# Performance work log

Measured on AMD Instinct MI355X. Metric: run time of the kernel, lower is better.

Reference implementation:

```python
import jax, jax.numpy as jnp
import numpy as np

B, T, D_MODEL = 2, 2048, 2048
N_HEADS, N_KV = 16, 8
HEAD_DIM = D_MODEL // N_HEADS  # 128
EPS = 1e-6


def rmsnorm(x, g):
    # qwen-compatible: compute in fp32, scale by learned weight
    xf = x.astype(jnp.float32)
    var = jnp.mean(xf * xf, axis=-1, keepdims=True)
    return (xf * jax.lax.rsqrt(var + EPS) * g).astype(x.dtype)


def apply_rope(x, cos, sin):
    # x: [b, h, t, d]; cos/sin: [t, d]
    d = x.shape[-1]
    x1, x2 = x[..., : d // 2], x[..., d // 2 :]
    rotated = jnp.concatenate([-x2, x1], axis=-1)
    return x * cos[None, None, :, :] + rotated * sin[None, None, :, :]


def setup_inputs() -> dict:
    key = jax.random.key(0)
    ks = jax.random.split(key, 8)
    x = jax.random.normal(ks[0], (B, T, D_MODEL), dtype=jnp.float32)
    # causal mask: True = masked out
    mask = jnp.triu(jnp.ones((T, T), dtype=bool), k=1)
    # rope tables
    inv_freq = 1.0 / (1e6 ** (np.arange(0, HEAD_DIM, 2, dtype=np.float32) / HEAD_DIM))
    angles = np.arange(T, dtype=np.float32)[:, None] * inv_freq[None, :]  # [T, d/2]
    angles = np.concatenate([angles, angles], axis=1)  # [T, d]
    cos = jnp.asarray(np.cos(angles), dtype=jnp.float32)
    sin = jnp.asarray(np.sin(angles), dtype=jnp.float32)
    s = 0.02
    Wq = jax.random.normal(ks[1], (D_MODEL, D_MODEL), dtype=jnp.float32) * s
    Wk = jax.random.normal(ks[2], (N_KV * HEAD_DIM, D_MODEL), dtype=jnp.float32) * s
    Wv = jax.random.normal(ks[3], (N_KV * HEAD_DIM, D_MODEL), dtype=jnp.float32) * s
    Wo = jax.random.normal(ks[4], (D_MODEL, D_MODEL), dtype=jnp.float32) * s
    bo = jnp.zeros((D_MODEL,), dtype=jnp.float32)
    gq = jnp.ones((HEAD_DIM,), dtype=jnp.float32)
    gk = jnp.ones((HEAD_DIM,), dtype=jnp.float32)
    return {"x": x, "mask": mask, "cos": cos, "sin": sin, "Wq": Wq, "Wk": Wk,
            "Wv": Wv, "Wo": Wo, "bo": bo, "gq": gq, "gk": gk}


def reference(x, mask, cos, sin, Wq, Wk, Wv, Wo, bo, gq, gk):
    b, t, _ = x.shape
    # projections
    q = (x @ Wq.T).reshape(b, t, N_HEADS, HEAD_DIM)
    q = rmsnorm(q, gq).transpose(0, 2, 1, 3)          # [b, H, t, d]
    q = apply_rope(q, cos[:t], sin[:t])
    k = (x @ Wk.T).reshape(b, t, N_KV, HEAD_DIM)
    k = rmsnorm(k, gk).transpose(0, 2, 1, 3)          # [b, G, t, d]
    k = apply_rope(k, cos[:t], sin[:t])
    v = (x @ Wv.T).reshape(b, t, N_KV, HEAD_DIM).transpose(0, 2, 1, 3)
    # GQA broadcast of KV heads
    rep = N_HEADS // N_KV
    k = jnp.repeat(k, rep, axis=1)                    # [b, H, t, d]
    v = jnp.repeat(v, rep, axis=1)
    scores = jnp.einsum("bhqd,bhkd->bhqk", q, k)
    scores = jnp.where(mask[:t, :t][None, None], -jnp.inf, scores)
    attn = jax.nn.softmax(scores / jnp.sqrt(jnp.float32(HEAD_DIM)), axis=-1)
    out = jnp.einsum("bhqk,bhkd->bqhd", attn, v).reshape(b, t, N_HEADS * HEAD_DIM)
    return out @ Wo.T + bo
```

## Files before the change

kernel.cpp:

```cpp
#include <hip/hip_runtime.h>
#include <stdint.h>

#define B_ 2
#define T_ 2048
#define DM 2048
#define NH 16
#define NKV 8
#define HD 128
#define NQKV 4096
#define SC2_ 0.12753102765f

typedef float fx4 __attribute__((ext_vector_type(4)));
typedef __bf16 bfx8 __attribute__((ext_vector_type(8)));
typedef unsigned short u16;
typedef unsigned int u32;

typedef __attribute__((address_space(1))) const void gas_t;
typedef __attribute__((address_space(3))) void las_t;

__device__ __forceinline__ u16 f2bf(float f) {
  u32 u = __float_as_uint(f);
  u = (u + 0x7fffu + ((u >> 16) & 1u)) >> 16;
  return (u16)u;
}

__device__ __forceinline__ void stage16(const void* g, void* l) {
  __builtin_amdgcn_global_load_lds((gas_t*)(uintptr_t)g, (las_t*)(uintptr_t)l,
                                   16, 0, 0);
}

__global__ void k_cvt(const float* __restrict__ in, u16* __restrict__ out, int n) {
  int i = (blockIdx.x * blockDim.x + threadIdx.x) * 4;
  if (i + 3 < n) {
    float4 v = *(const float4*)(in + i);
    u32 w0 = (u32)f2bf(v.x) | ((u32)f2bf(v.y) << 16);
    u32 w1 = (u32)f2bf(v.z) | ((u32)f2bf(v.w) << 16);
    *(uint2*)(out + i) = make_uint2(w0, w1);
  }
}

__global__ __launch_bounds__(512, 2) void k_gemm256(const u16* __restrict__ A,
                                                    const u16* __restrict__ Bm,
                                                    u16* __restrict__ C,
                                                    int M, int N, int K) {
  __shared__ __align__(16) u16 As[2][2][256 * 32];
  __shared__ __align__(16) u16 Bs[2][2][256 * 32];
  const int nbn = N >> 8;
  const int bm = blockIdx.x / nbn, bn = blockIdx.x % nbn;
  const int tid = threadIdx.x;
  const int w = tid >> 6, lane = tid & 63;
  const int wm = w >> 2, wn = w & 3;
  const int lr = lane & 15, lg = lane >> 4;
  const int cw = (lg ^ ((lr >> 1) & 3)) * 8;
  const u16* Ab = A + (size_t)bm * 256 * K;
  const u16* Bb = Bm + (size_t)bn * 256 * K;
  const int NT = K >> 6;

  auto stage = [&](const u16* gb, u16* region, int tile, int kh) {
#pragma unroll
    for (int i = 0; i < 2; i++) {
      int q = tid + i * 512;
      int row = q >> 2, ch = q & 3;
      int sc = ch ^ ((row >> 1) & 3);
      stage16(gb + (size_t)row * K + tile * 64 + kh * 32 + sc * 8, region + q * 8);
    }
  };

  fx4 acc[8][4];
  const fx4 zero4 = {0.f, 0.f, 0.f, 0.f};
#pragma unroll
  for (int m = 0; m < 8; m++)
#pragma unroll
    for (int n = 0; n < 4; n++) acc[m][n] = zero4;

  stage(Ab, &As[0][0][0], 0, 0);
  stage(Bb, &Bs[0][0][0], 0, 0);
  stage(Ab, &As[0][1][0], 0, 1);
  stage(Bb, &Bs[0][1][0], 0, 1);
  stage(Ab, &As[1][0][0], 1, 0);
  stage(Bb, &Bs[1][0][0], 1, 0);
  asm volatile("s_waitcnt vmcnt(4)" ::: "memory");
  __builtin_amdgcn_s_barrier();

  const int arow = (wm * 128 + lr) * 32;
  const int brow = (wn * 64 + lr) * 32;
  bfx8 af[4], bf[4];

#pragma unroll 1
  for (int t = 0; t < NT; t++) {
    const u16* A0 = &As[t & 1][0][0];
    const u16* A1 = &As[t & 1][1][0];
    const u16* B0 = &Bs[t & 1][0][0];
    const u16* B1 = &Bs[t & 1][1][0];
    const int p1 = (t + 1) & 1, p2 = t & 1;

#pragma unroll
    for (int mi = 0; mi < 4; mi++) af[mi] = *(const bfx8*)(A0 + arow + mi * 512 + cw);
#pragma unroll
    for (int n = 0; n < 4; n++) bf[n] = *(const bfx8*)(B0 + brow + n * 512 + cw);
    if (t + 1 < NT) stage(Ab, &As[p1][1][0], t + 1, 1);
    __builtin_amdgcn_s_barrier();
    asm volatile("s_waitcnt lgkmcnt(0)" ::: "memory");
    __builtin_amdgcn_sched_barrier(0);
    __builtin_amdgcn_s_setprio(1);
#pragma unroll
    for (int mi = 0; mi < 4; mi++)
#pragma unroll
      for (int n = 0; n < 4; n++)
        acc[mi][n] = __builtin_amdgcn_mfma_f32_16x16x32_bf16(af[mi], bf[n], acc[mi][n], 0, 0, 0);
    __builtin_amdgcn_s_setprio(0);
    __builtin_amdgcn_s_barrier();

#pragma unroll
    for (int mi = 0; mi < 4; mi++)
      af[mi] = *(const bfx8*)(A0 + arow + 2048 + mi * 512 + cw);
    if (t + 1 < NT) stage(Bb, &Bs[p1][1][0], t + 1, 1);
    __builtin_amdgcn_s_barrier();
    asm volatile("s_waitcnt lgkmcnt(0)" ::: "memory");
    __builtin_amdgcn_sched_barrier(0);
    __builtin_amdgcn_s_setprio(1);
#pragma unroll
    for (int mi = 0; mi < 4; mi++)
#pragma unroll
      for (int n = 0; n < 4; n++)
        acc[4 + mi][n] = __builtin_amdgcn_mfma_f32_16x16x32_bf16(af[mi], bf[n], acc[4 + mi][n], 0, 0, 0);
    __builtin_amdgcn_s_setprio(0);
    __builtin_amdgcn_s_barrier();

#pragma unroll
    for (int mi = 0; mi < 4; mi++) af[mi] = *(const bfx8*)(A1 + arow + mi * 512 + cw);
#pragma unroll
    for (int n = 0; n < 4; n++) bf[n] = *(const bfx8*)(B1 + brow + n * 512 + cw);
    if (t + 2 < NT) stage(Ab, &As[p2][0][0], t + 2, 0);
    __builtin_amdgcn_s_barrier();
    asm volatile("s_waitcnt lgkmcnt(0)" ::: "memory");
    __builtin_amdgcn_sched_barrier(0);
    __builtin_amdgcn_s_setprio(1);
#pragma unroll
    for (int mi = 0; mi < 4; mi++)
#pragma unroll
      for (int n = 0; n < 4; n++)
        acc[mi][n] = __builtin_amdgcn_mfma_f32_16x16x32_bf16(af[mi], bf[n], acc[mi][n], 0, 0, 0);
    __builtin_amdgcn_s_setprio(0);
    __builtin_amdgcn_s_barrier();

#pragma unroll
    for (int mi = 0; mi < 4; mi++)
      af[mi] = *(const bfx8*)(A1 + arow + 2048 + mi * 512 + cw);
    if (t + 2 < NT) stage(Bb, &Bs[p2][0][0], t + 2, 0);
    __builtin_amdgcn_s_barrier();
    asm volatile("s_waitcnt lgkmcnt(0)" ::: "memory");
    __builtin_amdgcn_sched_barrier(0);
    __builtin_amdgcn_s_setprio(1);
#pragma unroll
    for (int mi = 0; mi < 4; mi++)
#pragma unroll
      for (int n = 0; n < 4; n++)
        acc[4 + mi][n] = __builtin_amdgcn_mfma_f32_16x16x32_bf16(af[mi], bf[n], acc[4 + mi][n], 0, 0, 0);
    __builtin_amdgcn_s_setprio(0);
    asm volatile("s_waitcnt vmcnt(4)" ::: "memory");
    __builtin_amdgcn_s_barrier();
  }

  const int r0 = bm * 256 + wm * 128, c0 = bn * 256 + wn * 64;
#pragma unroll
  for (int m = 0; m < 8; m++) {
#pragma unroll
    for (int n = 0; n < 4; n++) {
      int c = c0 + n * 16 + lr;
#pragma unroll
      for (int i = 0; i < 4; i++)
        C[(size_t)(r0 + m * 16 + lg * 4 + i) * N + c] = f2bf(acc[m][n][i]);
    }
  }
}

template <bool OUT_F32>
__global__ __launch_bounds__(256, 2) void k_gemm(const u16* __restrict__ A,
                                                 const u16* __restrict__ Bm,
                                                 void* __restrict__ Cv,
                                                 const float* __restrict__ bias,
                                                 int M, int N, int K) {
  __shared__ __align__(16) u16 As[128 * 32];
  __shared__ __align__(16) u16 Bs[128 * 32];
  const int nbn = N >> 7;
  const int bm = blockIdx.x / nbn, bn = blockIdx.x % nbn;
  const int tid = threadIdx.x;
  const int w = tid >> 6, lane = tid & 63;
  const int wr = w >> 1, wc = w & 1;
  const int lr = lane & 15, lg = lane >> 4;
  const u16* Ab = A + (size_t)bm * 128 * K;
  const u16* Bb = Bm + (size_t)bn * 128 * K;
  const int srow = lane >> 2, skc = (lane & 3) * 8;

  fx4 zero4 = {0.f, 0.f, 0.f, 0.f};
  fx4 acc[4][4];
#pragma unroll
  for (int m = 0; m < 4; m++)
#pragma unroll
    for (int n = 0; n < 4; n++) acc[m][n] = zero4;

  for (int k0 = 0; k0 < K; k0 += 32) {
#pragma unroll
    for (int t = 0; t < 2; t++) {
      int s = w + t * 4;
      stage16(Ab + (size_t)(s * 16 + srow) * K + k0 + skc, As + s * 512 + lane * 8);
      stage16(Bb + (size_t)(s * 16 + srow) * K + k0 + skc, Bs + s * 512 + lane * 8);
    }
    __syncthreads();
    bfx8 af[4], bfr[4];
#pragma unroll
    for (int m = 0; m < 4; m++)
      af[m] = *(const bfx8*)(As + (wr * 64 + m * 16 + lr) * 32 + lg * 8);
#pragma unroll
    for (int n = 0; n < 4; n++)
      bfr[n] = *(const bfx8*)(Bs + (wc * 64 + n * 16 + lr) * 32 + lg * 8);
#pragma unroll
    for (int m = 0; m < 4; m++)
#pragma unroll
      for (int n = 0; n < 4; n++)
        acc[m][n] = __builtin_amdgcn_mfma_f32_16x16x32_bf16(af[m], bfr[n], acc[m][n], 0, 0, 0);
    __syncthreads();
  }

  const int r0 = bm * 128 + wr * 64, c0 = bn * 128 + wc * 64;
#pragma unroll
  for (int m = 0; m < 4; m++) {
#pragma unroll
    for (int n = 0; n < 4; n++) {
      int c = c0 + n * 16 + lr;
#pragma unroll
      for (int i = 0; i < 4; i++) {
        int r = r0 + m * 16 + lg * 4 + i;
        if (OUT_F32) {
          ((float*)Cv)[(size_t)r * N + c] = acc[m][n][i] + bias[c];
        } else {
          ((u16*)Cv)[(size_t)r * N + c] = f2bf(acc[m][n][i]);
        }
      }
    }
  }
}

__global__ __launch_bounds__(256) void k_qkpost(const u16* __restrict__ qkv,
                                                const float* __restrict__ cosp,
                                                const float* __restrict__ sinp,
                                                const float* __restrict__ gq,
                                                const float* __restrict__ gk,
                                                u16* __restrict__ Qo,
                                                u16* __restrict__ Ko) {
  int bi = blockIdx.x;
  int hh = bi % 24;
  int t64 = (bi / 24) % 32;
  int b = bi / 768;
  int tid = threadIdx.x;
  int j = tid >> 2, p = tid & 3;
  int t = t64 * 64 + j;
  bool isq = hh < 16;
  int colbase = isq ? hh * 128 : 2048 + (hh - 16) * 128;
  const u16* src = qkv + ((size_t)(b * T_ + t)) * NQKV + colbase + p * 32;

  float xv[32];
#pragma unroll
  for (int c = 0; c < 4; c++) {
    uint4 raw = *(const uint4*)(src + c * 8);
    u32 wd[4] = {raw.x, raw.y, raw.z, raw.w};
#pragma unroll
    for (int q2 = 0; q2 < 4; q2++) {
      xv[c * 8 + q2 * 2 + 0] = __uint_as_float(wd[q2] << 16);
      xv[c * 8 + q2 * 2 + 1] = __uint_as_float(wd[q2] & 0xffff0000u);
    }
  }
  float ss = 0.f;
#pragma unroll
  for (int i = 0; i < 32; i++) ss += xv[i] * xv[i];
  ss += __shfl_xor(ss, 1);
  ss += __shfl_xor(ss, 2);
  float rinv = rsqrtf(ss * (1.0f / 128.0f) + 1e-6f);
  const float* g = isq ? gq : gk;
  const float* cr = cosp + (size_t)t * 128 + p * 32;
  const float* sr = sinp + (size_t)t * 128 + p * 32;

  float ov[32];
#pragma unroll
  for (int i = 0; i < 32; i++) {
    float y = xv[i] * rinv * g[p * 32 + i];
    float oth = __shfl_xor(y, 2);
    float rot = (p < 2) ? -oth : oth;
    ov[i] = y * cr[i] + rot * sr[i];
  }

  uint4 pk[4];
#pragma unroll
  for (int c = 0; c < 4; c++) {
    u32 wd[4];
#pragma unroll
    for (int q2 = 0; q2 < 4; q2++)
      wd[q2] = (u32)f2bf(ov[c * 8 + q2 * 2]) | ((u32)f2bf(ov[c * 8 + q2 * 2 + 1]) << 16);
    pk[c] = make_uint4(wd[0], wd[1], wd[2], wd[3]);
  }

  if (isq) {
    u16* dst = Qo + (((size_t)(b * NH + hh)) * T_ + t) * HD + p * 32;
#pragma unroll
    for (int c = 0; c < 4; c++) *(uint4*)(dst + c * 8) = pk[c];
  } else {
    int hk = hh - 16;
    u16* dstrow = Ko + (((size_t)(b * NKV + hk)) * T_ + t) * HD;
#pragma unroll
    for (int c = 0; c < 4; c++) {
      int C = p * 4 + c;
      int Cs = C ^ (t & 7);
      *(uint4*)(dstrow + Cs * 8) = pk[c];
    }
  }
}

__global__ __launch_bounds__(256) void k_vtr(const u16* __restrict__ qkv,
                                             u16* __restrict__ vt) {
  __shared__ __align__(16) u16 sm[128 * 64];
  int bi = blockIdx.x;
  int hv = bi & 7;
  int t64 = (bi >> 3) & 31;
  int b = bi >> 8;
  int tid = threadIdx.x;
#pragma unroll
  for (int it = 0; it < 4; it++) {
    int idx = tid + it * 256;
    int tok = idx >> 4, c = idx & 15;
    uint4 raw = *(const uint4*)(qkv + ((size_t)(b * T_ + t64 * 64 + tok)) * NQKV +
                                3072 + hv * 128 + c * 8);
    u32 wd[4] = {raw.x, raw.y, raw.z, raw.w};
#pragma unroll
    for (int q2 = 0; q2 < 4; q2++) {
      sm[(c * 8 + q2 * 2 + 0) * 64 + tok] = (u16)(wd[q2] & 0xffffu);
      sm[(c * 8 + q2 * 2 + 1) * 64 + tok] = (u16)(wd[q2] >> 16);
    }
  }
  __syncthreads();
  int d = tid >> 1, half = tid & 1;
  size_t rowb = (((size_t)(b * NKV + hv)) * HD + d) * T_ + t64 * 64;
#pragma unroll
  for (int c = 0; c < 4; c++) {
    int cg = half * 4 + c;
    int cs = cg ^ (d & 7);
    u32 wd[4];
#pragma unroll
    for (int q2 = 0; q2 < 4; q2++) {
      u32 lo = sm[d * 64 + half * 32 + c * 8 + 2 * q2];
      u32 hi = sm[d * 64 + half * 32 + c * 8 + 2 * q2 + 1];
      wd[q2] = lo | (hi << 16);
    }
    *(uint4*)(vt + rowb + cs * 8) = make_uint4(wd[0], wd[1], wd[2], wd[3]);
  }
}

__global__ __launch_bounds__(512, 4) void k_attn(const u16* __restrict__ Qg,
                                                 const u16* __restrict__ Kg,
                                                 const u16* __restrict__ Vg,
                                                 u16* __restrict__ Og) {
  __shared__ __align__(16) u16 Ks[2][64 * 128];
  __shared__ __align__(16) u16 Vs[2][128 * 64];
  __shared__ __align__(16) u16 Ps[8][16 * 64];
  const int bi = blockIdx.x;
  const int zr = bi & 15, h = (bi >> 4) & 15, b = bi >> 8;
  const int z = b ? (15 - zr) : zr;
  const int hkv = h >> 1;
  const int tid = threadIdx.x, w = tid >> 6, lane = tid & 63;
  const int lr = lane & 15, lg = lane >> 4;
  const int zt = (w < 4) ? z : (31 - z);
  const int qr0 = zt * 64 + (w & 3) * 16;
  const int nch = 32 - z;
  const int myl = zt + 1;

  const u16* kb = Kg + ((size_t)(b * NKV + hkv)) * T_ * HD;
  const u16* vb = Vg + ((size_t)(b * NKV + hkv)) * HD * T_;
  u16* pw = &Ps[w][0];
  const fx4 zero4 = {0.f, 0.f, 0.f, 0.f};

  auto stageKV = [&](int buf, int kv0) {
    u16* Kd = &Ks[buf][0];
    u16* Vd = &Vs[buf][0];
#pragma unroll
    for (int it = 0; it < 2; it++) {
      int r = it * 32 + (tid >> 4);
      stage16(kb + (size_t)(kv0 + r) * HD + (tid & 15) * 8, Kd + it * 4096 + tid * 8);
      int d = it * 64 + (tid >> 3);
      stage16(vb + (size_t)d * T_ + kv0 + (tid & 7) * 8, Vd + it * 4096 + tid * 8);
    }
  };

  const u16* qbase = Qg + (((size_t)(b * NH + h)) * T_ + qr0 + lr) * HD;
  bfx8 qf[4];
#pragma unroll
  for (int kk = 0; kk < 4; kk++) qf[kk] = *(const bfx8*)(qbase + kk * 32 + lg * 8);

  fx4 o[8];
#pragma unroll
  for (int nf = 0; nf < 8; nf++) o[nf] = zero4;
  float l_i[4] = {0.f, 0.f, 0.f, 0.f};

  stageKV(0, 0);
  asm volatile("s_waitcnt vmcnt(0)" ::: "memory");
  __builtin_amdgcn_s_barrier();
  int cur = 0;

#pragma unroll 1
  for (int ch = 0; ch < nch; ch++) {
    if (ch + 1 < nch) {
      stageKV(cur ^ 1, (ch + 1) * 64);
      asm volatile("s_waitcnt vmcnt(4)" ::: "memory");
    } else {
      asm volatile("s_waitcnt vmcnt(0)" ::: "memory");
    }
    __builtin_amdgcn_s_barrier();

    if (ch < myl) {
      const u16* Kd = &Ks[cur][0];
      const u16* Vd = &Vs[cur][0];
      const int kv0 = ch * 64;
      const bool diag = (ch == zt);

      fx4 sa[4];
#pragma unroll
      for (int n = 0; n < 4; n++) sa[n] = zero4;
      __builtin_amdgcn_s_setprio(1);
#pragma unroll
      for (int n = 0; n < 4; n++) {
        const int kvl = n * 16 + lr;
        const u16* krow = Kd + kvl * 128;
#pragma unroll
        for (int kk = 0; kk < 4; kk++) {
          int cs = (kk * 4 + lg) ^ (kvl & 7);
          bfx8 kf = *(const bfx8*)(krow + cs * 8);
          sa[n] = __builtin_amdgcn_mfma_f32_16x16x32_bf16(qf[kk], kf, sa[n], 0, 0, 0);
        }
      }
      __builtin_amdgcn_s_setprio(0);

#pragma unroll
      for (int i = 0; i < 4; i++) {
        const int q = 4 * lg + i;
        const int r = qr0 + q;
        u16* prow = pw + q * 64;
#pragma unroll
        for (int n = 0; n < 4; n++) {
          float p = exp2f(sa[n][i] * SC2_);
          if (diag) p = ((kv0 + n * 16 + lr) > r) ? 0.f : p;
          l_i[i] += p;
          int chn = ((n * 2 + (lr >> 3)) ^ (q & 7));
          prow[chn * 8 + (lr & 7)] = f2bf(p);
        }
      }
      asm volatile("s_waitcnt lgkmcnt(0)" ::: "memory");

      bfx8 pa[2];
#pragma unroll
      for (int ks = 0; ks < 2; ks++) {
        int cp = (4 * ks + lg) ^ (lr & 7);
        pa[ks] = *(const bfx8*)(pw + lr * 64 + cp * 8);
      }
      __builtin_amdgcn_s_setprio(1);
#pragma unroll
      for (int nf = 0; nf < 8; nf++) {
        int d = nf * 16 + lr;
        const u16* vrow = Vd + d * 64;
#pragma unroll
        for (int ks = 0; ks < 2; ks++) {
          int cv = (4 * ks + lg) ^ (d & 7);
          bfx8 vf = *(const bfx8*)(vrow + cv * 8);
          o[nf] = __builtin_amdgcn_mfma_f32_16x16x32_bf16(pa[ks], vf, o[nf], 0, 0, 0);
        }
      }
      __builtin_amdgcn_s_setprio(0);
    }
    __builtin_amdgcn_s_barrier();
    cur ^= 1;
  }

  float inv[4];
#pragma unroll
  for (int i = 0; i < 4; i++) {
    float l = l_i[i];
    l += __shfl_xor(l, 1);
    l += __shfl_xor(l, 2);
    l += __shfl_xor(l, 4);
    l += __shfl_xor(l, 8);
    inv[i] = 1.0f / l;
  }
  u16* ob = Og + ((size_t)(b * T_ + qr0)) * DM + h * HD;
#pragma unroll
  for (int nf = 0; nf < 8; nf++)
#pragma unroll
    for (int i = 0; i < 4; i++)
      ob[(size_t)(4 * lg + i) * DM + nf * 16 + lr] = f2bf(o[nf][i] * inv[i]);
}

extern "C" void kernel_launch(void* const* d_in, const int* in_sizes, int n_in,
                              void* d_out, int out_size, void* d_ws, size_t ws_size,
                              hipStream_t stream) {
  const float* x = (const float*)d_in[0];
  const float* cosp = (const float*)d_in[2];
  const float* sinp = (const float*)d_in[3];
  const float* Wq = (const float*)d_in[4];
  const float* Wk = (const float*)d_in[5];
  const float* Wv = (const float*)d_in[6];
  const float* Wo = (const float*)d_in[7];
  const float* bo = (const float*)d_in[8];
  const float* gq = (const float*)d_in[9];
  const float* gk = (const float*)d_in[10];

  char* ws = (char*)d_ws;
  u16* xbf  = (u16*)(ws + 0);
  u16* wqkv = (u16*)(ws + 16777216);
  u16* wo   = (u16*)(ws + 33554432);
  u16* qkv  = (u16*)(ws + 41943040);
  u16* qb   = (u16*)(ws + 75497472);
  u16* kb   = (u16*)(ws + 92274688);
  u16* vt   = (u16*)(ws + 100663296);
  u16* ab   = (u16*)(ws + 109051904);
  float* out = (float*)d_out;

  k_cvt<<<8192, 256, 0, stream>>>(x, xbf, 8388608);
  k_cvt<<<4096, 256, 0, stream>>>(Wq, wqkv, 4194304);
  k_cvt<<<2048, 256, 0, stream>>>(Wk, wqkv + 4194304, 2097152);
  k_cvt<<<2048, 256, 0, stream>>>(Wv, wqkv + 6291456, 2097152);
  k_cvt<<<4096, 256, 0, stream>>>(Wo, wo, 4194304);

  k_gemm256<<<256, 512, 0, stream>>>(xbf, wqkv, qkv, 4096, 4096, 2048);
  k_qkpost<<<1536, 256, 0, stream>>>(qkv, cosp, sinp, gq, gk, qb, kb);
  k_vtr<<<512, 256, 0, stream>>>(qkv, vt);
  k_attn<<<512, 512, 0, stream>>>(qb, kb, vt, ab);
  k_gemm<true><<<512, 256, 0, stream>>>(ab, wo, out, bo, 4096, 2048, 2048);
}
```

Before: 248.8 us.

## Rewrite attention with 32x32 MFMA and register-resident P via permlane swap

The attention kernel moves from 16x16x32 to 32x32x16 bf16 MFMA tiles, with each wave owning 32 query rows, and the block shrinks from 512 to 256 threads. The computed S^T layout lets P be packed to bf16 and rearranged with v_permlane32_swap so it feeds the PV MFMA straight from registers, which removes the per-wave LDS round trip for P. Query-tile selection is also reshuffled across waves. The aim is less LDS traffic and fewer MFMA instructions, at the cost of more registers per wave and fewer waves per block sharing the same KV staging.

```diff
diff --git a/kernel.cpp b/kernel.cpp
--- a/kernel.cpp
+++ b/kernel.cpp
@@ -11,7 +11,9 @@
 #define SC2_ 0.12753102765f
 
 typedef float fx4 __attribute__((ext_vector_type(4)));
+typedef float fx16 __attribute__((ext_vector_type(16)));
 typedef __bf16 bfx8 __attribute__((ext_vector_type(8)));
+typedef unsigned int ux4 __attribute__((ext_vector_type(4)));
 typedef unsigned short u16;
 typedef unsigned int u32;
 
@@ -22,6 +24,9 @@
   u32 u = __float_as_uint(f);
   u = (u + 0x7fffu + ((u >> 16) & 1u)) >> 16;
   return (u16)u;
+}
+__device__ __forceinline__ u32 pk2bf(float lo, float hi) {
+  return (u32)f2bf(lo) | ((u32)f2bf(hi) << 16);
 }
 
 __device__ __forceinline__ void stage16(const void* g, void* l) {
@@ -355,50 +360,52 @@
   }
 }
 
-__global__ __launch_bounds__(512, 4) void k_attn(const u16* __restrict__ Qg,
+__global__ __launch_bounds__(256, 2) void k_attn(const u16* __restrict__ Qg,
                                                  const u16* __restrict__ Kg,
                                                  const u16* __restrict__ Vg,
                                                  u16* __restrict__ Og) {
   __shared__ __align__(16) u16 Ks[2][64 * 128];
   __shared__ __align__(16) u16 Vs[2][128 * 64];
-  __shared__ __align__(16) u16 Ps[8][16 * 64];
   const int bi = blockIdx.x;
   const int zr = bi & 15, h = (bi >> 4) & 15, b = bi >> 8;
   const int z = b ? (15 - zr) : zr;
   const int hkv = h >> 1;
   const int tid = threadIdx.x, w = tid >> 6, lane = tid & 63;
-  const int lr = lane & 15, lg = lane >> 4;
-  const int zt = (w < 4) ? z : (31 - z);
-  const int qr0 = zt * 64 + (w & 3) * 16;
+  const int q31 = lane & 31, H8 = lane >> 5;
+  const int sel = ((w >> 1) ^ bi) & 1;
+  const int zt = sel ? (31 - z) : z;
+  const int qr0 = zt * 64 + (w & 1) * 32;
+  const int qg = qr0 + q31;
   const int nch = 32 - z;
   const int myl = zt + 1;
 
   const u16* kb = Kg + ((size_t)(b * NKV + hkv)) * T_ * HD;
   const u16* vb = Vg + ((size_t)(b * NKV + hkv)) * HD * T_;
-  u16* pw = &Ps[w][0];
-  const fx4 zero4 = {0.f, 0.f, 0.f, 0.f};
+
+  const u16* qrow = Qg + (((size_t)(b * NH + h)) * T_ + qg) * HD;
+  bfx8 qf[8];
+#pragma unroll
+  for (int step = 0; step < 8; step++)
+    qf[step] = *(const bfx8*)(qrow + step * 16 + H8 * 8);
+
+  fx16 o[4];
+  const fx16 zero16 = {0.f, 0.f, 0.f, 0.f, 0.f, 0.f, 0.f, 0.f,
+                       0.f, 0.f, 0.f, 0.f, 0.f, 0.f, 0.f, 0.f};
+#pragma unroll
+  for (int db = 0; db < 4; db++) o[db] = zero16;
+  float l_i = 0.f;
 
   auto stageKV = [&](int buf, int kv0) {
     u16* Kd = &Ks[buf][0];
     u16* Vd = &Vs[buf][0];
 #pragma unroll
-    for (int it = 0; it < 2; it++) {
-      int r = it * 32 + (tid >> 4);
-      stage16(kb + (size_t)(kv0 + r) * HD + (tid & 15) * 8, Kd + it * 4096 + tid * 8);
-      int d = it * 64 + (tid >> 3);
-      stage16(vb + (size_t)d * T_ + kv0 + (tid & 7) * 8, Vd + it * 4096 + tid * 8);
+    for (int it = 0; it < 4; it++) {
+      int r = it * 16 + (tid >> 4);
+      stage16(kb + (size_t)(kv0 + r) * HD + (tid & 15) * 8, Kd + it * 2048 + tid * 8);
+      int d = it * 32 + (tid >> 3);
+      stage16(vb + (size_t)d * T_ + kv0 + (tid & 7) * 8, Vd + it * 2048 + tid * 8);
     }
   };
-
-  const u16* qbase = Qg + (((size_t)(b * NH + h)) * T_ + qr0 + lr) * HD;
-  bfx8 qf[4];
-#pragma unroll
-  for (int kk = 0; kk < 4; kk++) qf[kk] = *(const bfx8*)(qbase + kk * 32 + lg * 8);
-
-  fx4 o[8];
-#pragma unroll
-  for (int nf = 0; nf < 8; nf++) o[nf] = zero4;
-  float l_i[4] = {0.f, 0.f, 0.f, 0.f};
 
   stageKV(0, 0);
   asm volatile("s_waitcnt vmcnt(0)" ::: "memory");
@@ -409,7 +416,7 @@
   for (int ch = 0; ch < nch; ch++) {
     if (ch + 1 < nch) {
       stageKV(cur ^ 1, (ch + 1) * 64);
-      asm volatile("s_waitcnt vmcnt(4)" ::: "memory");
+      asm volatile("s_waitcnt vmcnt(8)" ::: "memory");
     } else {
       asm volatile("s_waitcnt vmcnt(0)" ::: "memory");
     }
@@ -421,79 +428,73 @@
       const int kv0 = ch * 64;
       const bool diag = (ch == zt);
 
-      fx4 sa[4];
-#pragma unroll
-      for (int n = 0; n < 4; n++) sa[n] = zero4;
-      __builtin_amdgcn_s_setprio(1);
-#pragma unroll
-      for (int n = 0; n < 4; n++) {
-        const int kvl = n * 16 + lr;
-        const u16* krow = Kd + kvl * 128;
-#pragma unroll
-        for (int kk = 0; kk < 4; kk++) {
-          int cs = (kk * 4 + lg) ^ (kvl & 7);
-          bfx8 kf = *(const bfx8*)(krow + cs * 8);
-          sa[n] = __builtin_amdgcn_mfma_f32_16x16x32_bf16(qf[kk], kf, sa[n], 0, 0, 0);
+#pragma unroll
+      for (int kvb = 0; kvb < 2; kvb++) {
+        const int krow = kvb * 32 + q31;
+        const u16* kr = Kd + krow * 128;
+        fx16 st = zero16;
+        __builtin_amdgcn_s_setprio(1);
+#pragma unroll
+        for (int step = 0; step < 8; step++) {
+          int cs = ((step << 1) | H8) ^ (krow & 7);
+          bfx8 kf = *(const bfx8*)(kr + cs * 8);
+          st = __builtin_amdgcn_mfma_f32_32x32x16_bf16(kf, qf[step], st, 0, 0, 0);
+        }
+        __builtin_amdgcn_s_setprio(0);
+
+        float pv[16];
+#pragma unroll
+        for (int r = 0; r < 16; r++) {
+          float p = exp2f(st[r] * SC2_);
+          if (diag) {
+            int kvg = kv0 + kvb * 32 + (r & 3) + 8 * (r >> 2) + 4 * H8;
+            p = (kvg > qg) ? 0.f : p;
+          }
+          l_i += p;
+          pv[r] = p;
+        }
+
+#pragma unroll
+        for (int half = 0; half < 2; half++) {
+          const int rb = half * 8;
+          u32 A0 = pk2bf(pv[rb + 0], pv[rb + 1]);
+          u32 A1 = pk2bf(pv[rb + 2], pv[rb + 3]);
+          u32 B0 = pk2bf(pv[rb + 4], pv[rb + 5]);
+          u32 B1 = pk2bf(pv[rb + 6], pv[rb + 7]);
+          asm volatile("v_permlane32_swap_b32 %0, %1" : "+v"(A0), "+v"(B0));
+          asm volatile("v_permlane32_swap_b32 %0, %1" : "+v"(A1), "+v"(B1));
+          union { ux4 u; bfx8 b; } pa;
+          pa.u = (ux4){A0, A1, B0, B1};
+          const int ks = kvb * 2 + half;
+          __builtin_amdgcn_s_setprio(1);
+#pragma unroll
+          for (int db = 0; db < 4; db++) {
+            int vrow = db * 32 + q31;
+            int cv = ((ks << 1) | H8) ^ (vrow & 7);
+            bfx8 vf = *(const bfx8*)(Vd + vrow * 64 + cv * 8);
+            o[db] = __builtin_amdgcn_mfma_f32_32x32x16_bf16(vf, pa.b, o[db], 0, 0, 0);
+          }
+          __builtin_amdgcn_s_setprio(0);
         }
       }
-      __builtin_amdgcn_s_setprio(0);
-
-#pragma unroll
-      for (int i = 0; i < 4; i++) {
-        const int q = 4 * lg + i;
-        const int r = qr0 + q;
-        u16* prow = pw + q * 64;
-#pragma unroll
-        for (int n = 0; n < 4; n++) {
-          float p = exp2f(sa[n][i] * SC2_);
-          if (diag) p = ((kv0 + n * 16 + lr) > r) ? 0.f : p;
-          l_i[i] += p;
-          int chn = ((n * 2 + (lr >> 3)) ^ (q & 7));
-          prow[chn * 8 + (lr & 7)] = f2bf(p);
-        }
-      }
-      asm volatile("s_waitcnt lgkmcnt(0)" ::: "memory");
-
-      bfx8 pa[2];
-#pragma unroll
-      for (int ks = 0; ks < 2; ks++) {
-        int cp = (4 * ks + lg) ^ (lr & 7);
-        pa[ks] = *(const bfx8*)(pw + lr * 64 + cp * 8);
-      }
-      __builtin_amdgcn_s_setprio(1);
-#pragma unroll
-      for (int nf = 0; nf < 8; nf++) {
-        int d = nf * 16 + lr;
-        const u16* vrow = Vd + d * 64;
-#pragma unroll
-        for (int ks = 0; ks < 2; ks++) {
-          int cv = (4 * ks + lg) ^ (d & 7);
-          bfx8 vf = *(const bfx8*)(vrow + cv * 8);
-          o[nf] = __builtin_amdgcn_mfma_f32_16x16x32_bf16(pa[ks], vf, o[nf], 0, 0, 0);
-        }
-      }
-      __builtin_amdgcn_s_setprio(0);
     }
     __builtin_amdgcn_s_barrier();
     cur ^= 1;
   }
 
-  float inv[4];
-#pragma unroll
-  for (int i = 0; i < 4; i++) {
-    float l = l_i[i];
-    l += __shfl_xor(l, 1);
-    l += __shfl_xor(l, 2);
-    l += __shfl_xor(l, 4);
-    l += __shfl_xor(l, 8);
-    inv[i] = 1.0f / l;
-  }
-  u16* ob = Og + ((size_t)(b * T_ + qr0)) * DM + h * HD;
-#pragma unroll
-  for (int nf = 0; nf < 8; nf++)
-#pragma unroll
-    for (int i = 0; i < 4; i++)
-      ob[(size_t)(4 * lg + i) * DM + nf * 16 + lr] = f2bf(o[nf][i] * inv[i]);
+  float lt = l_i + __shfl_xor(l_i, 32);
+  float inv = 1.0f / lt;
+  u16* ob = Og + ((size_t)(b * T_ + qg)) * DM + h * HD;
+#pragma unroll
+  for (int db = 0; db < 4; db++) {
+#pragma unroll
+    for (int g = 0; g < 4; g++) {
+      int d0 = db * 32 + 8 * g + 4 * H8;
+      u32 w0 = pk2bf(o[db][4 * g + 0] * inv, o[db][4 * g + 1] * inv);
+      u32 w1 = pk2bf(o[db][4 * g + 2] * inv, o[db][4 * g + 3] * inv);
+      *(uint2*)(ob + d0) = make_uint2(w0, w1);
+    }
+  }
 }
 
 extern "C" void kernel_launch(void* const* d_in, const int* in_sizes, int n_in,
@@ -530,6 +531,6 @@
   k_gemm256<<<256, 512, 0, stream>>>(xbf, wqkv, qkv, 4096, 4096, 2048);
   k_qkpost<<<1536, 256, 0, stream>>>(qkv, cosp, sinp, gq, gk, qb, kb);
   k_vtr<<<512, 256, 0, stream>>>(qkv, vt);
-  k_attn<<<512, 512, 0, stream>>>(qb, kb, vt, ab);
+  k_attn<<<512, 256, 0, stream>>>(qb, kb, vt, ab);
   k_gemm<true><<<512, 256, 0, stream>>>(ab, wo, out, bo, 4096, 2048, 2048);
 }
```

Result: slower. 267.2 us (+7.4%).

## Pipeline output projection GEMM with double-buffered swizzled LDS and async prefetch

Applied to the files above, without the earlier changes.

Replaces the simple synchronous output-projection GEMM with a version modelled on the 256-tile QKV GEMM. It uses double-buffered LDS tiles with K split in halves, an XOR-swizzled LDS layout, and staged global prefetch interleaved with the MFMA phases. This is meant to overlap the global loads with compute and to cut bank conflicts and barrier stalls. It also adds a full vmcnt(0) drain on the last iterations of both GEMMs so no loads are left outstanding at the tail. The cost is a larger LDS footprint of 64KB per block, which may limit occupancy at two blocks per CU.

```diff
diff --git a/kernel.cpp b/kernel.cpp
--- a/kernel.cpp
+++ b/kernel.cpp
@@ -158,7 +158,11 @@
       for (int n = 0; n < 4; n++)
         acc[4 + mi][n] = __builtin_amdgcn_mfma_f32_16x16x32_bf16(af[mi], bf[n], acc[4 + mi][n], 0, 0, 0);
     __builtin_amdgcn_s_setprio(0);
-    asm volatile("s_waitcnt vmcnt(4)" ::: "memory");
+    if (t + 2 < NT) {
+      asm volatile("s_waitcnt vmcnt(4)" ::: "memory");
+    } else {
+      asm volatile("s_waitcnt vmcnt(0)" ::: "memory");
+    }
     __builtin_amdgcn_s_barrier();
   }
 
@@ -175,69 +179,143 @@
   }
 }
 
-template <bool OUT_F32>
-__global__ __launch_bounds__(256, 2) void k_gemm(const u16* __restrict__ A,
-                                                 const u16* __restrict__ Bm,
-                                                 void* __restrict__ Cv,
-                                                 const float* __restrict__ bias,
-                                                 int M, int N, int K) {
-  __shared__ __align__(16) u16 As[128 * 32];
-  __shared__ __align__(16) u16 Bs[128 * 32];
+__global__ __launch_bounds__(256, 2) void k_gemmo(const u16* __restrict__ A,
+                                                  const u16* __restrict__ Bm,
+                                                  float* __restrict__ C,
+                                                  const float* __restrict__ bias,
+                                                  int M, int N, int K) {
+  __shared__ __align__(16) u16 As[2][2][128 * 32];
+  __shared__ __align__(16) u16 Bs[2][2][128 * 32];
   const int nbn = N >> 7;
   const int bm = blockIdx.x / nbn, bn = blockIdx.x % nbn;
   const int tid = threadIdx.x;
   const int w = tid >> 6, lane = tid & 63;
-  const int wr = w >> 1, wc = w & 1;
+  const int wm = w >> 1, wn = w & 1;
   const int lr = lane & 15, lg = lane >> 4;
+  const int cw = (lg ^ ((lr >> 1) & 3)) * 8;
   const u16* Ab = A + (size_t)bm * 128 * K;
   const u16* Bb = Bm + (size_t)bn * 128 * K;
-  const int srow = lane >> 2, skc = (lane & 3) * 8;
-
-  fx4 zero4 = {0.f, 0.f, 0.f, 0.f};
+  const int NT = K >> 6;
+
+  auto stage = [&](const u16* gb, u16* region, int tile, int kh) {
+#pragma unroll
+    for (int i = 0; i < 2; i++) {
+      int q = tid + i * 256;
+      int row = q >> 2, ch = q & 3;
+      int sc = ch ^ ((row >> 1) & 3);
+      stage16(gb + (size_t)row * K + tile * 64 + kh * 32 + sc * 8, region + q * 8);
+    }
+  };
+
   fx4 acc[4][4];
+  const fx4 zero4 = {0.f, 0.f, 0.f, 0.f};
 #pragma unroll
   for (int m = 0; m < 4; m++)
 #pragma unroll
     for (int n = 0; n < 4; n++) acc[m][n] = zero4;
 
-  for (int k0 = 0; k0 < K; k0 += 32) {
-#pragma unroll
-    for (int t = 0; t < 2; t++) {
-      int s = w + t * 4;
-      stage16(Ab + (size_t)(s * 16 + srow) * K + k0 + skc, As + s * 512 + lane * 8);
-      stage16(Bb + (size_t)(s * 16 + srow) * K + k0 + skc, Bs + s * 512 + lane * 8);
-    }
-    __syncthreads();
-    bfx8 af[4], bfr[4];
-#pragma unroll
-    for (int m = 0; m < 4; m++)
-      af[m] = *(const bfx8*)(As + (wr * 64 + m * 16 + lr) * 32 + lg * 8);
-#pragma unroll
-    for (int n = 0; n < 4; n++)
-      bfr[n] = *(const bfx8*)(Bs + (wc * 64 + n * 16 + lr) * 32 + lg * 8);
-#pragma unroll
-    for (int m = 0; m < 4; m++)
-#pragma unroll
-      for (int n = 0; n < 4; n++)
-        acc[m][n] = __builtin_amdgcn_mfma_f32_16x16x32_bf16(af[m], bfr[n], acc[m][n], 0, 0, 0);
-    __syncthreads();
-  }
-
-  const int r0 = bm * 128 + wr * 64, c0 = bn * 128 + wc * 64;
+  stage(Ab, &As[0][0][0], 0, 0);
+  stage(Bb, &Bs[0][0][0], 0, 0);
+  stage(Ab, &As[0][1][0], 0, 1);
+  stage(Bb, &Bs[0][1][0], 0, 1);
+  stage(Ab, &As[1][0][0], 1, 0);
+  stage(Bb, &Bs[1][0][0], 1, 0);
+  asm volatile("s_waitcnt vmcnt(4)" ::: "memory");
+  __builtin_amdgcn_s_barrier();
+
+  const int arow = (wm * 64 + lr) * 32;
+  const int brow = (wn * 64 + lr) * 32;
+  bfx8 af[2], bf[4];
+
+#pragma unroll 1
+  for (int t = 0; t < NT; t++) {
+    const u16* A0 = &As[t & 1][0][0];
+    const u16* A1 = &As[t & 1][1][0];
+    const u16* B0 = &Bs[t & 1][0][0];
+    const u16* B1 = &Bs[t & 1][1][0];
+    const int p1 = (t + 1) & 1, p2 = t & 1;
+
+#pragma unroll
+    for (int mi = 0; mi < 2; mi++) af[mi] = *(const bfx8*)(A0 + arow + mi * 512 + cw);
+#pragma unroll
+    for (int n = 0; n < 4; n++) bf[n] = *(const bfx8*)(B0 + brow + n * 512 + cw);
+    if (t + 1 < NT) stage(Ab, &As[p1][1][0], t + 1, 1);
+    __builtin_amdgcn_s_barrier();
+    asm volatile("s_waitcnt lgkmcnt(0)" ::: "memory");
+    __builtin_amdgcn_sched_barrier(0);
+    __builtin_amdgcn_s_setprio(1);
+#pragma unroll
+    for (int mi = 0; mi < 2; mi++)
+#pragma unroll
+      for (int n = 0; n < 4; n++)
+        acc[mi][n] = __builtin_amdgcn_mfma_f32_16x16x32_bf16(af[mi], bf[n], acc[mi][n], 0, 0, 0);
+    __builtin_amdgcn_s_setprio(0);
+    __builtin_amdgcn_s_barrier();
+
+#pragma unroll
+    for (int mi = 0; mi < 2; mi++)
+      af[mi] = *(const bfx8*)(A0 + arow + 1024 + mi * 512 + cw);
+    if (t + 1 < NT) stage(Bb, &Bs[p1][1][0], t + 1, 1);
+    __builtin_amdgcn_s_barrier();
+    asm volatile("s_waitcnt lgkmcnt(0)" ::: "memory");
+    __builtin_amdgcn_sched_barrier(0);
+    __builtin_amdgcn_s_setprio(1);
+#pragma unroll
+    for (int mi = 0; mi < 2; mi++)
+#pragma unroll
+      for (int n = 0; n < 4; n++)
+        acc[2 + mi][n] = __builtin_amdgcn_mfma_f32_16x16x32_bf16(af[mi], bf[n], acc[2 + mi][n], 0, 0, 0);
+    __builtin_amdgcn_s_setprio(0);
+    __builtin_amdgcn_s_barrier();
+
+#pragma unroll
+    for (int mi = 0; mi < 2; mi++) af[mi] = *(const bfx8*)(A1 + arow + mi * 512 + cw);
+#pragma unroll
+    for (int n = 0; n < 4; n++) bf[n] = *(const bfx8*)(B1 + brow + n * 512 + cw);
+    if (t + 2 < NT) stage(Ab, &As[p2][0][0], t + 2, 0);
+    __builtin_amdgcn_s_barrier();
+    asm volatile("s_waitcnt lgkmcnt(0)" ::: "memory");
+    __builtin_amdgcn_sched_barrier(0);
+    __builtin_amdgcn_s_setprio(1);
+#pragma unroll
+    for (int mi = 0; mi < 2; mi++)
+#pragma unroll
+      for (int n = 0; n < 4; n++)
+        acc[mi][n] = __builtin_amdgcn_mfma_f32_16x16x32_bf16(af[mi], bf[n], acc[mi][n], 0, 0, 0);
+    __builtin_amdgcn_s_setprio(0);
+    __builtin_amdgcn_s_barrier();
+
+#pragma unroll
+    for (int mi = 0; mi < 2; mi++)
+      af[mi] = *(const bfx8*)(A1 + arow + 1024 + mi * 512 + cw);
+    if (t + 2 < NT) stage(Bb, &Bs[p2][0][0], t + 2, 0);
+    __builtin_amdgcn_s_barrier();
+    asm volatile("s_waitcnt lgkmcnt(0)" ::: "memory");
+    __builtin_amdgcn_sched_barrier(0);
+    __builtin_amdgcn_s_setprio(1);
+#pragma unroll
+    for (int mi = 0; mi < 2; mi++)
+#pragma unroll
+      for (int n = 0; n < 4; n++)
+        acc[2 + mi][n] = __builtin_amdgcn_mfma_f32_16x16x32_bf16(af[mi], bf[n], acc[2 + mi][n], 0, 0, 0);
+    __builtin_amdgcn_s_setprio(0);
+    if (t + 2 < NT) {
+      asm volatile("s_waitcnt vmcnt(4)" ::: "memory");
+    } else {
+      asm volatile("s_waitcnt vmcnt(0)" ::: "memory");
+    }
+    __builtin_amdgcn_s_barrier();
+  }
+
+  const int r0 = bm * 128 + wm * 64, c0 = bn * 128 + wn * 64;
 #pragma unroll
   for (int m = 0; m < 4; m++) {
 #pragma unroll
     for (int n = 0; n < 4; n++) {
       int c = c0 + n * 16 + lr;
 #pragma unroll
-      for (int i = 0; i < 4; i++) {
-        int r = r0 + m * 16 + lg * 4 + i;
-        if (OUT_F32) {
-          ((float*)Cv)[(size_t)r * N + c] = acc[m][n][i] + bias[c];
-        } else {
-          ((u16*)Cv)[(size_t)r * N + c] = f2bf(acc[m][n][i]);
-        }
-      }
+      for (int i = 0; i < 4; i++)
+        C[(size_t)(r0 + m * 16 + lg * 4 + i) * N + c] = acc[m][n][i] + bias[c];
     }
   }
 }
@@ -531,5 +609,5 @@
   k_qkpost<<<1536, 256, 0, stream>>>(qkv, cosp, sinp, gq, gk, qb, kb);
   k_vtr<<<512, 256, 0, stream>>>(qkv, vt);
   k_attn<<<512, 512, 0, stream>>>(qb, kb, vt, ab);
-  k_gemm<true><<<512, 256, 0, stream>>>(ab, wo, out, bo, 4096, 2048, 2048);
-}
+  k_gemmo<<<512, 256, 0, stream>>>(ab, wo, out, bo, 4096, 2048, 2048);
+}
```

Measured after the change: 243.3 us. 1.02x faster.
